# Kernel tuning notes

Hardware: AMD Instinct MI355X
Metric: run time of the kernel (lower is better)

The kernel has to match this reference:

```python
import jax, jax.numpy as jnp
import numpy as np

B, C, H, W = 4, 256, 64, 64
CH = C // 2  # inner channels of the non-local block


def _conv1x1(x, w, b):
    # 1x1 conv == channel-mixing einsum; x: [B,C,H,W], w: [O,C], b: [O]
    return jnp.einsum('oc,bchw->bohw', w, x) + b[None, :, None, None]


def setup_inputs() -> dict:
    key = jax.random.key(0)
    ks = jax.random.split(key, 9)
    s = 0.02  # small init so exp(scores) stays in fp32 range (no max-subtraction in this block)
    return {
        'x':  jax.random.normal(ks[0], (B, C, H, W), dtype=jnp.float32),
        'w1': s * jax.random.normal(ks[1], (CH, C), dtype=jnp.float32),
        'b1': jnp.zeros((CH,), jnp.float32),
        'w2': s * jax.random.normal(ks[2], (CH, C), dtype=jnp.float32),
        'b2': jnp.zeros((CH,), jnp.float32),
        'w3': s * jax.random.normal(ks[3], (CH, C), dtype=jnp.float32),
        'b3': jnp.zeros((CH,), jnp.float32),
        'w4': s * jax.random.normal(ks[4], (C, CH), dtype=jnp.float32),
        'b4': jnp.zeros((C,), jnp.float32),
    }


def reference(x, w1, b1, w2, b2, w3, b3, w4, b4):
    b, c, h, w = x.shape
    n = h * w
    theta = _conv1x1(x, w1, b1).reshape(b, -1, n)  # [B, C/2, N]
    phi   = _conv1x1(x, w2, b2).reshape(b, -1, n)  # [B, C/2, N]
    g     = _conv1x1(x, w3, b3).reshape(b, -1, n)  # [B, C/2, N]
    # full non-local affinity: [B, N, N]
    scores = jnp.einsum('bci,bcj->bij', theta, phi)
    attn = jnp.exp(scores)  # faithful: no max-subtraction in the original
    attn = attn / jnp.sum(attn, axis=1, keepdims=True)  # normalize over dim=1 as written
    y = jnp.einsum('bij,bcj->bci', attn, g)  # [B, C/2, N]
    y = y.reshape(b, -1, h, w)               # [B, C/2, H, W]
    out = _conv1x1(y, w4, b4) + x            # project back to C, residual
    return out
```

## Files before the change

kernel.cpp:

```cpp
#include <hip/hip_runtime.h>

#define DEVI __device__ __forceinline__

typedef __attribute__((ext_vector_type(8))) short bf16x8;
typedef __attribute__((ext_vector_type(4))) short bf16x4;
typedef __attribute__((ext_vector_type(4))) float f32x4;

#define MFMA16 __builtin_amdgcn_mfma_f32_16x16x32_bf16

DEVI short f2bs(float f) {
  union { float f; unsigned u; } v; v.f = f;
  unsigned r = v.u + 0x7fffu + ((v.u >> 16) & 1u);
  return (short)(r >> 16);
}
DEVI float bs2f(short s) {
  union { unsigned u; float f; } v; v.u = ((unsigned)(unsigned short)s) << 16;
  return v.f;
}

DEVI void gload_lds16(const short* g, short* lds) {
  __builtin_amdgcn_global_load_lds(
      (const __attribute__((address_space(1))) unsigned int*)g,
      (__attribute__((address_space(3))) unsigned int*)lds, 16, 0, 0);
}

DEVI void stage_chunk(short* lds, const short* g, int ldg, int tid) {
#pragma unroll
  for (int it = 0; it < 2; ++it) {
    int slot = it * 256 + tid;
    int row  = slot >> 2;
    int ko   = (slot & 3) << 3;
    gload_lds16(g + (size_t)row * ldg + ko, lds + slot * 8);
  }
}

DEVI void stage_chunk64(short* lds, const short* g, int ldg, int tid) {
  int row = tid >> 2, ko = (tid & 3) << 3;
  gload_lds16(g + (size_t)row * ldg + ko, lds + tid * 8);
}

DEVI bf16x8 lds8(const short* p) { return *(const bf16x8*)p; }

DEVI void zero_acc(f32x4 (&a)[4][4]) {
  f32x4 z = {0.f, 0.f, 0.f, 0.f};
#pragma unroll
  for (int i = 0; i < 4; ++i)
#pragma unroll
    for (int j = 0; j < 4; ++j) a[i][j] = z;
}

__global__ __launch_bounds__(256) void k_transpose_cast(const float* __restrict__ x,
                                                        short* __restrict__ xt) {
  __shared__ float t[64][65];
  int b = blockIdx.z;
  int c0 = blockIdx.y * 64;
  int p0 = blockIdx.x * 64;
  int tid = threadIdx.x;
  const float* xb = x + (size_t)b * 256 * 4096;
#pragma unroll
  for (int i = 0; i < 16; ++i) {
    int idx = i * 256 + tid;
    int c = idx >> 6, p = idx & 63;
    t[p][c] = xb[(size_t)(c0 + c) * 4096 + p0 + p];
  }
  __syncthreads();
  short* xtb = xt + ((size_t)b * 4096 + p0) * 256 + c0;
#pragma unroll
  for (int i = 0; i < 16; ++i) {
    int idx = i * 256 + tid;
    int p = idx >> 6, c = idx & 63;
    xtb[(size_t)p * 256 + c] = f2bs(t[p][c]);
  }
}

__global__ __launch_bounds__(256) void k_cast_w(const float* __restrict__ w1,
                                                const float* __restrict__ w2,
                                                const float* __restrict__ w3,
                                                short* __restrict__ w123) {
  int i = blockIdx.x * 256 + threadIdx.x;
  if (i < 384 * 256) {
    int r = i >> 8;
    const float* w = (r < 128) ? w1 : (r < 256 ? w2 : w3);
    w123[i] = f2bs(w[(size_t)(r & 127) * 256 + (i & 255)]);
  }
}

__global__ __launch_bounds__(256) void k_proj(const short* __restrict__ xt,
                                              const short* __restrict__ w123,
                                              const float* __restrict__ b1,
                                              const float* __restrict__ b2,
                                              const float* __restrict__ b3,
                                              short* __restrict__ theta,
                                              short* __restrict__ phi,
                                              short* __restrict__ gbuf) {
  __shared__ short aL[128 * 32];
  __shared__ short bL[128 * 32];
  __shared__ short oL[128 * 136];
  int tid = threadIdx.x;
  int m0 = blockIdx.x * 128;
  int nb = blockIdx.y;
  int b  = blockIdx.z;
  int lane = tid & 63, wid = tid >> 6;
  int col = lane & 15, quad = lane >> 4;
  int wm = (wid >> 1) * 64, wn = (wid & 1) * 64;
  const short* A = xt + ((size_t)b * 4096 + m0) * 256;
  const short* B = w123 + (size_t)nb * 128 * 256;
  f32x4 acc[4][4];
  zero_acc(acc);
  for (int ks = 0; ks < 8; ++ks) {
    __syncthreads();
    stage_chunk(aL, A + ks * 32, 256, tid);
    stage_chunk(bL, B + ks * 32, 256, tid);
    __syncthreads();
    bf16x8 af[4], bf_[4];
#pragma unroll
    for (int mi = 0; mi < 4; ++mi) af[mi] = lds8(&aL[(wm + mi * 16 + col) * 32 + quad * 8]);
#pragma unroll
    for (int ni = 0; ni < 4; ++ni) bf_[ni] = lds8(&bL[(wn + ni * 16 + col) * 32 + quad * 8]);
#pragma unroll
    for (int mi = 0; mi < 4; ++mi)
#pragma unroll
      for (int ni = 0; ni < 4; ++ni)
        acc[mi][ni] = MFMA16(af[mi], bf_[ni], acc[mi][ni], 0, 0, 0);
  }
  const float* bias = (nb == 0) ? b1 : (nb == 1 ? b2 : b3);
  __syncthreads();
#pragma unroll
  for (int mi = 0; mi < 4; ++mi)
#pragma unroll
    for (int ni = 0; ni < 4; ++ni) {
      float bv = bias[wn + ni * 16 + col];
#pragma unroll
      for (int r = 0; r < 4; ++r)
        oL[(wm + mi * 16 + quad * 4 + r) * 136 + wn + ni * 16 + col] = f2bs(acc[mi][ni][r] + bv);
    }
  __syncthreads();
  short* O = ((nb == 0) ? theta : (nb == 1) ? phi : gbuf) + ((size_t)b * 4096 + m0) * 128;
#pragma unroll
  for (int it = 0; it < 8; ++it) {
    int slot = it * 256 + tid;
    int r = slot >> 4, cp = (slot & 15) * 8;
    *(bf16x8*)(O + (size_t)r * 128 + cp) = lds8(&oL[r * 136 + cp]);
  }
}

__global__ __launch_bounds__(256, 2) void k_denom(const short* __restrict__ theta,
                                                  const short* __restrict__ phi,
                                                  float* __restrict__ dpart) {
  __shared__ short phB[2][16384];
  __shared__ float part[1024];
  int tid = threadIdx.x;
  int ib = blockIdx.x, jc = blockIdx.y, b = blockIdx.z;
  int lane = tid & 63, wid = tid >> 6;
  int col = lane & 15, quad = lane >> 4;
  int wm = (wid >> 1) * 64, wn = (wid & 1) * 64;
  const short* T = theta + ((size_t)b * 4096 + ib * 128) * 128;
  const short* P = phi + ((size_t)b * 4096 + (size_t)jc * 1024) * 128;
  short* Lb = &phB[0][0];
#pragma unroll
  for (int ks = 0; ks < 4; ++ks) stage_chunk(Lb + ks * 8192, T + ks * 32, 128, tid);
  __syncthreads();
  bf16x8 ath[4][4];
#pragma unroll
  for (int ks = 0; ks < 4; ++ks)
#pragma unroll
    for (int mi = 0; mi < 4; ++mi)
      ath[ks][mi] = lds8(&Lb[ks * 8192 + (wm + mi * 16 + col) * 32 + quad * 8]);
  __syncthreads();
#pragma unroll
  for (int ks = 0; ks < 4; ++ks) stage_chunk(&phB[0][0] + ks * 4096, P + ks * 32, 128, tid);
  for (int jt = 0; jt < 8; ++jt) {
    int cur = jt & 1;
    __syncthreads();
    if (jt < 7) {
      const short* Pn = P + (size_t)(jt + 1) * 128 * 128;
#pragma unroll
      for (int ks = 0; ks < 4; ++ks) stage_chunk(&phB[cur ^ 1][0] + ks * 4096, Pn + ks * 32, 128, tid);
    }
    f32x4 sacc[4][4];
    zero_acc(sacc);
#pragma unroll
    for (int ks = 0; ks < 4; ++ks) {
      bf16x8 bp[4];
#pragma unroll
      for (int ni = 0; ni < 4; ++ni) bp[ni] = lds8(&phB[cur][ks * 4096 + (wn + ni * 16 + col) * 32 + quad * 8]);
#pragma unroll
      for (int mi = 0; mi < 4; ++mi)
#pragma unroll
        for (int ni = 0; ni < 4; ++ni)
          sacc[mi][ni] = MFMA16(ath[ks][mi], bp[ni], sacc[mi][ni], 0, 0, 0);
    }
#pragma unroll
    for (int ni = 0; ni < 4; ++ni) {
      float s = 0.f;
#pragma unroll
      for (int mi = 0; mi < 4; ++mi)
#pragma unroll
        for (int r = 0; r < 4; ++r) s += __expf(sacc[mi][ni][r]);
      part[((wid >> 1) * 4 + quad) * 128 + wn + ni * 16 + col] = s;
    }
    __syncthreads();
    if (tid < 128) {
      float d = 0.f;
#pragma unroll
      for (int q = 0; q < 8; ++q) d += part[q * 128 + tid];
      dpart[((size_t)(b * 32 + ib)) * 4096 + jc * 1024 + jt * 128 + tid] = d;
    }
  }
}

__global__ __launch_bounds__(256) void k_fold(const short* __restrict__ gbuf,
                                              const float* __restrict__ dpart,
                                              short* __restrict__ gprime) {
  __shared__ float dinv[128];
  __shared__ short t[128 * 136];
  int tid = threadIdx.x;
  int jb = blockIdx.x, b = blockIdx.y;
  int j0 = jb * 128;
  if (tid < 128) {
    float d = 0.f;
    for (int ib = 0; ib < 32; ++ib) d += dpart[((size_t)(b * 32 + ib)) * 4096 + j0 + tid];
    dinv[tid] = 1.0f / d;
  }
  __syncthreads();
  const short* G = gbuf + ((size_t)b * 4096 + j0) * 128;
#pragma unroll
  for (int it = 0; it < 8; ++it) {
    int slot = it * 256 + tid;
    int j = slot >> 4, c8 = (slot & 15) * 8;
    bf16x8 gv = *(const bf16x8*)(G + (size_t)j * 128 + c8);
    float di = dinv[j];
#pragma unroll
    for (int e = 0; e < 8; ++e) t[(c8 + e) * 136 + j] = f2bs(bs2f(gv[e]) * di);
  }
  __syncthreads();
  short* GP = gprime + (size_t)b * 128 * 4096 + j0;
#pragma unroll
  for (int it = 0; it < 8; ++it) {
    int slot = it * 256 + tid;
    int c = slot >> 4, j8 = (slot & 15) * 8;
    *(bf16x8*)(GP + (size_t)c * 4096 + j8) = *(const bf16x8*)&t[c * 136 + j8];
  }
}

__global__ __launch_bounds__(256, 2) void k_attn_pv(const short* __restrict__ theta,
                                                    const short* __restrict__ phi,
                                                    const short* __restrict__ gprime,
                                                    short* __restrict__ ypart) {
  __shared__ short L[40960];
  int tid = threadIdx.x;
  int ib = blockIdx.x, jc = blockIdx.y, b = blockIdx.z;
  int lane = tid & 63, wid = tid >> 6;
  int col = lane & 15, quad = lane >> 4;
  int wm = (wid >> 1) * 64;
  int wnS = (wid & 1) * 32;
  int wnV = (wid & 1) * 64;
  const short* T = theta + ((size_t)b * 4096 + ib * 128) * 128;
  const short* PH = phi + ((size_t)b * 4096 + (size_t)jc * 1024) * 128;
  const short* GP = gprime + (size_t)b * 128 * 4096 + jc * 1024;
  short* pP = L + 32768;
#pragma unroll
  for (int ks = 0; ks < 4; ++ks) stage_chunk(L + ks * 8192, T + ks * 32, 128, tid);
  __syncthreads();
  bf16x8 ath[4][4];
#pragma unroll
  for (int ks = 0; ks < 4; ++ks)
#pragma unroll
    for (int mi = 0; mi < 4; ++mi)
      ath[ks][mi] = lds8(&L[ks * 8192 + (wm + mi * 16 + col) * 32 + quad * 8]);
  __syncthreads();
#pragma unroll
  for (int ks = 0; ks < 4; ++ks) stage_chunk64(L + ks * 2048, PH + ks * 32, 128, tid);
#pragma unroll
  for (int jh = 0; jh < 2; ++jh) stage_chunk(L + 16384 + jh * 4096, GP + jh * 32, 4096, tid);
  f32x4 accy[4][4];
  zero_acc(accy);
  for (int jt = 0; jt < 16; ++jt) {
    int cur = jt & 1;
    short* phc = L + cur * 8192;
    short* phn = L + (cur ^ 1) * 8192;
    short* gpc = L + 16384 + cur * 8192;
    short* gpn = L + 16384 + (cur ^ 1) * 8192;
    __syncthreads();
    if (jt < 15) {
      const short* PHn = PH + (size_t)(jt + 1) * 64 * 128;
#pragma unroll
      for (int ks = 0; ks < 4; ++ks) stage_chunk64(phn + ks * 2048, PHn + ks * 32, 128, tid);
    }
    f32x4 s[4][2];
#pragma unroll
    for (int mi = 0; mi < 4; ++mi)
#pragma unroll
      for (int ni = 0; ni < 2; ++ni) s[mi][ni] = (f32x4){0.f, 0.f, 0.f, 0.f};
#pragma unroll
    for (int ks = 0; ks < 4; ++ks) {
      bf16x8 bp[2];
#pragma unroll
      for (int ni = 0; ni < 2; ++ni) bp[ni] = lds8(&phc[ks * 2048 + (wnS + ni * 16 + col) * 32 + quad * 8]);
#pragma unroll
      for (int mi = 0; mi < 4; ++mi)
#pragma unroll
        for (int ni = 0; ni < 2; ++ni)
          s[mi][ni] = MFMA16(ath[ks][mi], bp[ni], s[mi][ni], 0, 0, 0);
    }
#pragma unroll
    for (int mi = 0; mi < 4; ++mi)
#pragma unroll
      for (int ni = 0; ni < 2; ++ni) {
        int jj = wnS + ni * 16 + col;
        int cj = jj >> 5, jg = (jj >> 3) & 3, jl = jj & 7;
#pragma unroll
        for (int r = 0; r < 4; ++r) {
          int i = wm + mi * 16 + quad * 4 + r;
          pP[cj * 4096 + i * 32 + (((jg ^ (i >> 2)) & 3) << 3) + jl] = f2bs(__expf(s[mi][ni][r]));
        }
      }
    __syncthreads();
    if (jt < 15) {
      const short* GPn = GP + (jt + 1) * 64;
#pragma unroll
      for (int jh = 0; jh < 2; ++jh) stage_chunk(gpn + jh * 4096, GPn + jh * 32, 4096, tid);
    }
#pragma unroll
    for (int ks = 0; ks < 2; ++ks) {
      bf16x8 ap[4], bg[4];
#pragma unroll
      for (int mi = 0; mi < 4; ++mi) {
        int i = wm + mi * 16 + col;
        ap[mi] = lds8(&pP[ks * 4096 + i * 32 + (((quad ^ (i >> 2)) & 3) << 3)]);
      }
#pragma unroll
      for (int ni = 0; ni < 4; ++ni) bg[ni] = lds8(&gpc[ks * 4096 + (wnV + ni * 16 + col) * 32 + quad * 8]);
#pragma unroll
      for (int mi = 0; mi < 4; ++mi)
#pragma unroll
        for (int ni = 0; ni < 4; ++ni)
          accy[mi][ni] = MFMA16(ap[mi], bg[ni], accy[mi][ni], 0, 0, 0);
    }
  }
  short* Yp = ypart + ((size_t)(jc * 4 + b) * 4096 + (size_t)ib * 128) * 128;
#pragma unroll
  for (int half = 0; half < 2; ++half) {
    __syncthreads();
    if ((wid >> 1) == half) {
#pragma unroll
      for (int mi = 0; mi < 4; ++mi)
#pragma unroll
        for (int ni = 0; ni < 4; ++ni)
#pragma unroll
          for (int r = 0; r < 4; ++r)
            pP[(mi * 16 + quad * 4 + r) * 128 + wnV + ni * 16 + col] = f2bs(accy[mi][ni][r]);
    }
    __syncthreads();
#pragma unroll
    for (int it = 0; it < 4; ++it) {
      int slot = it * 256 + tid;
      int r = slot >> 4, c8 = (slot & 15) * 8;
      *(bf16x8*)(Yp + (size_t)(half * 64 + r) * 128 + c8) = lds8(&pP[r * 128 + c8]);
    }
  }
}

__global__ __launch_bounds__(256) void k_out(const short* __restrict__ ypart,
                                             const float* __restrict__ w4,
                                             const float* __restrict__ b4,
                                             const float* __restrict__ x,
                                             float* __restrict__ out) {
  __shared__ short wL[4 * 4096];
  __shared__ short yL[4 * 4096];
  __shared__ float bLs[128];
  int tid = threadIdx.x;
  int ibk = blockIdx.x, ob = blockIdx.y, b = blockIdx.z;
  int o0 = ob * 128, i0 = ibk * 128;
  int lane = tid & 63, wid = tid >> 6;
  int col = lane & 15, quad = lane >> 4;
  int wm = (wid >> 1) * 64, wn = (wid & 1) * 64;
#pragma unroll
  for (int it = 0; it < 16; ++it) {
    int slot = it * 256 + tid;
    int r = slot >> 5, c4 = (slot & 31) * 4;
    int ks = c4 >> 5, cr = c4 & 31;
    f32x4 wv = *(const f32x4*)(w4 + (size_t)(o0 + r) * 128 + c4);
    bf16x4 wp;
#pragma unroll
    for (int e = 0; e < 4; ++e) wp[e] = f2bs(wv[e]);
    *(bf16x4*)&wL[ks * 4096 + r * 32 + cr] = wp;
  }
#pragma unroll
  for (int it = 0; it < 8; ++it) {
    int slot = it * 256 + tid;
    int r = slot >> 4, c8 = (slot & 15) * 8;
    int ks = c8 >> 5, cr = c8 & 31;
    float a8[8];
#pragma unroll
    for (int e = 0; e < 8; ++e) a8[e] = 0.f;
#pragma unroll
    for (int p = 0; p < 4; ++p) {
      bf16x8 v = *(const bf16x8*)(ypart + ((size_t)(p * 4 + b) * 4096 + i0 + r) * 128 + c8);
#pragma unroll
      for (int e = 0; e < 8; ++e) a8[e] += bs2f(v[e]);
    }
    bf16x8 yv;
#pragma unroll
    for (int e = 0; e < 8; ++e) yv[e] = f2bs(a8[e]);
    *(bf16x8*)&yL[ks * 4096 + r * 32 + cr] = yv;
  }
  if (tid < 128) bLs[tid] = b4[o0 + tid];
  __syncthreads();
  f32x4 acc[4][4];
  zero_acc(acc);
#pragma unroll
  for (int ks = 0; ks < 4; ++ks) {
    bf16x8 af[4], bf_[4];
#pragma unroll
    for (int mi = 0; mi < 4; ++mi) af[mi] = lds8(&wL[ks * 4096 + (wm + mi * 16 + col) * 32 + quad * 8]);
#pragma unroll
    for (int ni = 0; ni < 4; ++ni) bf_[ni] = lds8(&yL[ks * 4096 + (wn + ni * 16 + col) * 32 + quad * 8]);
#pragma unroll
    for (int mi = 0; mi < 4; ++mi)
#pragma unroll
      for (int ni = 0; ni < 4; ++ni)
        acc[mi][ni] = MFMA16(af[mi], bf_[ni], acc[mi][ni], 0, 0, 0);
  }
  const float* X = x + ((size_t)b * 256 + o0) * 4096 + i0;
  float* O = out + ((size_t)b * 256 + o0) * 4096 + i0;
#pragma unroll
  for (int mi = 0; mi < 4; ++mi)
#pragma unroll
    for (int ni = 0; ni < 4; ++ni)
#pragma unroll
      for (int r = 0; r < 4; ++r) {
        int o = wm + mi * 16 + quad * 4 + r;
        int i = wn + ni * 16 + col;
        O[(size_t)o * 4096 + i] = acc[mi][ni][r] + X[(size_t)o * 4096 + i] + bLs[o];
      }
}

extern "C" void kernel_launch(void* const* d_in, const int* in_sizes, int n_in,
                              void* d_out, int out_size, void* d_ws, size_t ws_size,
                              hipStream_t stream) {
  const float* x  = (const float*)d_in[0];
  const float* w1 = (const float*)d_in[1];
  const float* b1 = (const float*)d_in[2];
  const float* w2 = (const float*)d_in[3];
  const float* b2 = (const float*)d_in[4];
  const float* w3 = (const float*)d_in[5];
  const float* b3 = (const float*)d_in[6];
  const float* w4 = (const float*)d_in[7];
  const float* b4 = (const float*)d_in[8];
  char* ws = (char*)d_ws;
  short* xt     = (short*)(ws + 0);
  short* w123   = (short*)(ws + 8388608);
  short* theta  = (short*)(ws + 8585216);
  short* phi    = (short*)(ws + 12779520);
  short* gbuf   = (short*)(ws + 16973824);
  short* gprime = (short*)(ws + 21168128);
  float* dpart  = (float*)(ws + 25362432);
  short* ypart  = (short*)(ws + 27459584);
  float* out    = (float*)d_out;
  (void)in_sizes; (void)n_in; (void)out_size; (void)ws_size;

  k_transpose_cast<<<dim3(64, 4, 4), dim3(256), 0, stream>>>(x, xt);
  k_cast_w<<<dim3(384), dim3(256), 0, stream>>>(w1, w2, w3, w123);
  k_proj<<<dim3(32, 3, 4), dim3(256), 0, stream>>>(xt, w123, b1, b2, b3, theta, phi, gbuf);
  k_denom<<<dim3(32, 4, 4), dim3(256), 0, stream>>>(theta, phi, dpart);
  k_fold<<<dim3(32, 4), dim3(256), 0, stream>>>(gbuf, dpart, gprime);
  k_attn_pv<<<dim3(32, 4, 4), dim3(256), 0, stream>>>(theta, phi, gprime, ypart);
  k_out<<<dim3(32, 2, 4), dim3(256), 0, stream>>>(ypart, w4, b4, x, out);
}
```

Baseline: 174.9 us.

## Fuse prep kernels, drop fold pass, apply column normalization inside attention

Merges the input transpose-cast and the weight cast into one launch. The projection kernel now writes g already transposed, so the separate fold kernel goes away. The denominator kernel reduces column sums with warp shuffles and atomically accumulates into a small zeroed buffer instead of writing per-block partials. The attention kernel reads those sums and scales exp(scores) by their reciprocal before the PV matmul. The aim is fewer launches and less intermediate traffic, at the cost of atomics, a memset, and extra per-tile normalization work and barriers in the attention loop.

```diff
diff --git a/kernel.cpp b/kernel.cpp
--- a/kernel.cpp
+++ b/kernel.cpp
@@ -49,13 +49,26 @@
     for (int j = 0; j < 4; ++j) a[i][j] = z;
 }
 
-__global__ __launch_bounds__(256) void k_transpose_cast(const float* __restrict__ x,
-                                                        short* __restrict__ xt) {
+__global__ __launch_bounds__(256) void k_prep(const float* __restrict__ x,
+                                              const float* __restrict__ w1,
+                                              const float* __restrict__ w2,
+                                              const float* __restrict__ w3,
+                                              short* __restrict__ xt,
+                                              short* __restrict__ w123) {
+  int tid = threadIdx.x;
+  if (blockIdx.y == 4) {
+    int lin = blockIdx.z * 64 + blockIdx.x;
+    for (int i = lin * 256 + tid; i < 384 * 256; i += 65536) {
+      int r = i >> 8;
+      const float* w = (r < 128) ? w1 : (r < 256 ? w2 : w3);
+      w123[i] = f2bs(w[(size_t)(r & 127) * 256 + (i & 255)]);
+    }
+    return;
+  }
   __shared__ float t[64][65];
   int b = blockIdx.z;
   int c0 = blockIdx.y * 64;
   int p0 = blockIdx.x * 64;
-  int tid = threadIdx.x;
   const float* xb = x + (size_t)b * 256 * 4096;
 #pragma unroll
   for (int i = 0; i < 16; ++i) {
@@ -70,18 +83,6 @@
     int idx = i * 256 + tid;
     int p = idx >> 6, c = idx & 63;
     xtb[(size_t)p * 256 + c] = f2bs(t[p][c]);
-  }
-}
-
-__global__ __launch_bounds__(256) void k_cast_w(const float* __restrict__ w1,
-                                                const float* __restrict__ w2,
-                                                const float* __restrict__ w3,
-                                                short* __restrict__ w123) {
-  int i = blockIdx.x * 256 + threadIdx.x;
-  if (i < 384 * 256) {
-    int r = i >> 8;
-    const float* w = (r < 128) ? w1 : (r < 256 ? w2 : w3);
-    w123[i] = f2bs(w[(size_t)(r & 127) * 256 + (i & 255)]);
   }
 }
 
@@ -92,7 +93,7 @@
                                               const float* __restrict__ b3,
                                               short* __restrict__ theta,
                                               short* __restrict__ phi,
-                                              short* __restrict__ gbuf) {
+                                              short* __restrict__ gT) {
   __shared__ short aL[128 * 32];
   __shared__ short bL[128 * 32];
   __shared__ short oL[128 * 136];
@@ -125,231 +126,222 @@
   }
   const float* bias = (nb == 0) ? b1 : (nb == 1 ? b2 : b3);
   __syncthreads();
-#pragma unroll
-  for (int mi = 0; mi < 4; ++mi)
-#pragma unroll
-    for (int ni = 0; ni < 4; ++ni) {
-      float bv = bias[wn + ni * 16 + col];
-#pragma unroll
-      for (int r = 0; r < 4; ++r)
-        oL[(wm + mi * 16 + quad * 4 + r) * 136 + wn + ni * 16 + col] = f2bs(acc[mi][ni][r] + bv);
-    }
-  __syncthreads();
-  short* O = ((nb == 0) ? theta : (nb == 1) ? phi : gbuf) + ((size_t)b * 4096 + m0) * 128;
-#pragma unroll
-  for (int it = 0; it < 8; ++it) {
-    int slot = it * 256 + tid;
-    int r = slot >> 4, cp = (slot & 15) * 8;
-    *(bf16x8*)(O + (size_t)r * 128 + cp) = lds8(&oL[r * 136 + cp]);
+  if (nb < 2) {
+#pragma unroll
+    for (int mi = 0; mi < 4; ++mi)
+#pragma unroll
+      for (int ni = 0; ni < 4; ++ni) {
+        float bv = bias[wn + ni * 16 + col];
+#pragma unroll
+        for (int r = 0; r < 4; ++r)
+          oL[(wm + mi * 16 + quad * 4 + r) * 136 + wn + ni * 16 + col] = f2bs(acc[mi][ni][r] + bv);
+      }
+    __syncthreads();
+    short* O = ((nb == 0) ? theta : phi) + ((size_t)b * 4096 + m0) * 128;
+#pragma unroll
+    for (int it = 0; it < 8; ++it) {
+      int slot = it * 256 + tid;
+      int r = slot >> 4, cp = (slot & 15) * 8;
+      *(bf16x8*)(O + (size_t)r * 128 + cp) = lds8(&oL[r * 136 + cp]);
+    }
+  } else {
+#pragma unroll
+    for (int mi = 0; mi < 4; ++mi)
+#pragma unroll
+      for (int ni = 0; ni < 4; ++ni) {
+        float bv = bias[wn + ni * 16 + col];
+#pragma unroll
+        for (int r = 0; r < 4; ++r)
+          oL[(wn + ni * 16 + col) * 136 + wm + mi * 16 + quad * 4 + r] = f2bs(acc[mi][ni][r] + bv);
+      }
+    __syncthreads();
+    short* O = gT + (size_t)b * 128 * 4096 + m0;
+#pragma unroll
+    for (int it = 0; it < 8; ++it) {
+      int slot = it * 256 + tid;
+      int c = slot >> 4, p8 = (slot & 15) * 8;
+      *(bf16x8*)(O + (size_t)c * 4096 + p8) = lds8(&oL[c * 136 + p8]);
+    }
   }
 }
 
 __global__ __launch_bounds__(256, 2) void k_denom(const short* __restrict__ theta,
                                                   const short* __restrict__ phi,
-                                                  float* __restrict__ dpart) {
-  __shared__ short phB[2][16384];
-  __shared__ float part[1024];
+                                                  float* __restrict__ dsum) {
+  __shared__ short L[16384];
   int tid = threadIdx.x;
   int ib = blockIdx.x, jc = blockIdx.y, b = blockIdx.z;
   int lane = tid & 63, wid = tid >> 6;
   int col = lane & 15, quad = lane >> 4;
-  int wm = (wid >> 1) * 64, wn = (wid & 1) * 64;
-  const short* T = theta + ((size_t)b * 4096 + ib * 128) * 128;
-  const short* P = phi + ((size_t)b * 4096 + (size_t)jc * 1024) * 128;
-  short* Lb = &phB[0][0];
-#pragma unroll
-  for (int ks = 0; ks < 4; ++ks) stage_chunk(Lb + ks * 8192, T + ks * 32, 128, tid);
-  __syncthreads();
-  bf16x8 ath[4][4];
+  int wmj = (wid & 1) * 32;
+  int wni = (wid >> 1) * 64;
+  const short* TH = theta + ((size_t)b * 4096 + ib * 128) * 128;
+  const short* PH = phi + ((size_t)b * 4096 + (size_t)jc * 1024) * 128;
+  float* D = dsum + b * 4096 + jc * 1024;
+#pragma unroll
+  for (int ks = 0; ks < 4; ++ks) stage_chunk(L + ks * 4096, TH + ks * 32, 128, tid);
+  __syncthreads();
+  bf16x8 bth[4][4];
 #pragma unroll
   for (int ks = 0; ks < 4; ++ks)
 #pragma unroll
-    for (int mi = 0; mi < 4; ++mi)
-      ath[ks][mi] = lds8(&Lb[ks * 8192 + (wm + mi * 16 + col) * 32 + quad * 8]);
-  __syncthreads();
-#pragma unroll
-  for (int ks = 0; ks < 4; ++ks) stage_chunk(&phB[0][0] + ks * 4096, P + ks * 32, 128, tid);
-  for (int jt = 0; jt < 8; ++jt) {
-    int cur = jt & 1;
-    __syncthreads();
-    if (jt < 7) {
-      const short* Pn = P + (size_t)(jt + 1) * 128 * 128;
-#pragma unroll
-      for (int ks = 0; ks < 4; ++ks) stage_chunk(&phB[cur ^ 1][0] + ks * 4096, Pn + ks * 32, 128, tid);
-    }
-    f32x4 sacc[4][4];
-    zero_acc(sacc);
+    for (int ni = 0; ni < 4; ++ni)
+      bth[ks][ni] = lds8(&L[ks * 4096 + (wni + ni * 16 + col) * 32 + quad * 8]);
+  __syncthreads();
+#pragma unroll
+  for (int ks = 0; ks < 4; ++ks) stage_chunk64(L + ks * 2048, PH + ks * 32, 128, tid);
+  for (int jt = 0; jt < 16; ++jt) {
+    short* phc = L + (jt & 1) * 8192;
+    short* phn = L + ((jt & 1) ^ 1) * 8192;
+    __syncthreads();
+    if (jt < 15) {
+      const short* PHn = PH + (size_t)(jt + 1) * 64 * 128;
+#pragma unroll
+      for (int ks = 0; ks < 4; ++ks) stage_chunk64(phn + ks * 2048, PHn + ks * 32, 128, tid);
+    }
+    f32x4 s[2][4];
+#pragma unroll
+    for (int mi = 0; mi < 2; ++mi)
+#pragma unroll
+      for (int ni = 0; ni < 4; ++ni) s[mi][ni] = (f32x4){0.f, 0.f, 0.f, 0.f};
 #pragma unroll
     for (int ks = 0; ks < 4; ++ks) {
-      bf16x8 bp[4];
-#pragma unroll
-      for (int ni = 0; ni < 4; ++ni) bp[ni] = lds8(&phB[cur][ks * 4096 + (wn + ni * 16 + col) * 32 + quad * 8]);
-#pragma unroll
-      for (int mi = 0; mi < 4; ++mi)
+      bf16x8 ap[2];
+#pragma unroll
+      for (int mi = 0; mi < 2; ++mi) ap[mi] = lds8(&phc[ks * 2048 + (wmj + mi * 16 + col) * 32 + quad * 8]);
+#pragma unroll
+      for (int mi = 0; mi < 2; ++mi)
 #pragma unroll
         for (int ni = 0; ni < 4; ++ni)
-          sacc[mi][ni] = MFMA16(ath[ks][mi], bp[ni], sacc[mi][ni], 0, 0, 0);
-    }
-#pragma unroll
-    for (int ni = 0; ni < 4; ++ni) {
-      float s = 0.f;
-#pragma unroll
-      for (int mi = 0; mi < 4; ++mi)
-#pragma unroll
-        for (int r = 0; r < 4; ++r) s += __expf(sacc[mi][ni][r]);
-      part[((wid >> 1) * 4 + quad) * 128 + wn + ni * 16 + col] = s;
-    }
-    __syncthreads();
-    if (tid < 128) {
-      float d = 0.f;
-#pragma unroll
-      for (int q = 0; q < 8; ++q) d += part[q * 128 + tid];
-      dpart[((size_t)(b * 32 + ib)) * 4096 + jc * 1024 + jt * 128 + tid] = d;
-    }
-  }
-}
-
-__global__ __launch_bounds__(256) void k_fold(const short* __restrict__ gbuf,
-                                              const float* __restrict__ dpart,
-                                              short* __restrict__ gprime) {
-  __shared__ float dinv[128];
-  __shared__ short t[128 * 136];
-  int tid = threadIdx.x;
-  int jb = blockIdx.x, b = blockIdx.y;
-  int j0 = jb * 128;
-  if (tid < 128) {
-    float d = 0.f;
-    for (int ib = 0; ib < 32; ++ib) d += dpart[((size_t)(b * 32 + ib)) * 4096 + j0 + tid];
-    dinv[tid] = 1.0f / d;
-  }
-  __syncthreads();
-  const short* G = gbuf + ((size_t)b * 4096 + j0) * 128;
-#pragma unroll
-  for (int it = 0; it < 8; ++it) {
-    int slot = it * 256 + tid;
-    int j = slot >> 4, c8 = (slot & 15) * 8;
-    bf16x8 gv = *(const bf16x8*)(G + (size_t)j * 128 + c8);
-    float di = dinv[j];
-#pragma unroll
-    for (int e = 0; e < 8; ++e) t[(c8 + e) * 136 + j] = f2bs(bs2f(gv[e]) * di);
-  }
-  __syncthreads();
-  short* GP = gprime + (size_t)b * 128 * 4096 + j0;
-#pragma unroll
-  for (int it = 0; it < 8; ++it) {
-    int slot = it * 256 + tid;
-    int c = slot >> 4, j8 = (slot & 15) * 8;
-    *(bf16x8*)(GP + (size_t)c * 4096 + j8) = *(const bf16x8*)&t[c * 136 + j8];
-  }
-}
-
-__global__ __launch_bounds__(256, 2) void k_attn_pv(const short* __restrict__ theta,
-                                                    const short* __restrict__ phi,
-                                                    const short* __restrict__ gprime,
-                                                    short* __restrict__ ypart) {
-  __shared__ short L[40960];
+          s[mi][ni] = MFMA16(ap[mi], bth[ks][ni], s[mi][ni], 0, 0, 0);
+    }
+#pragma unroll
+    for (int mi = 0; mi < 2; ++mi)
+#pragma unroll
+      for (int r = 0; r < 4; ++r) {
+        float ps = __expf(s[mi][0][r]) + __expf(s[mi][1][r]) +
+                   __expf(s[mi][2][r]) + __expf(s[mi][3][r]);
+        ps += __shfl_xor(ps, 1, 16);
+        ps += __shfl_xor(ps, 2, 16);
+        ps += __shfl_xor(ps, 4, 16);
+        ps += __shfl_xor(ps, 8, 16);
+        if (col == 0) atomicAdd(D + jt * 64 + wmj + mi * 16 + quad * 4 + r, ps);
+      }
+  }
+}
+
+__global__ __launch_bounds__(256, 2) void k_attn(const short* __restrict__ theta,
+                                                 const short* __restrict__ phi,
+                                                 const short* __restrict__ gT,
+                                                 const float* __restrict__ dsum,
+                                                 short* __restrict__ ypart) {
+  __shared__ short L[33280];
   int tid = threadIdx.x;
   int ib = blockIdx.x, jc = blockIdx.y, b = blockIdx.z;
   int lane = tid & 63, wid = tid >> 6;
   int col = lane & 15, quad = lane >> 4;
-  int wm = (wid >> 1) * 64;
-  int wnS = (wid & 1) * 32;
-  int wnV = (wid & 1) * 64;
-  const short* T = theta + ((size_t)b * 4096 + ib * 128) * 128;
+  int wmj = (wid & 1) * 32;
+  int wni = (wid >> 1) * 64;
+  int wmi = (wid >> 1) * 64;
+  int wnc = (wid & 1) * 64;
+  const short* TH = theta + ((size_t)b * 4096 + ib * 128) * 128;
   const short* PH = phi + ((size_t)b * 4096 + (size_t)jc * 1024) * 128;
-  const short* GP = gprime + (size_t)b * 128 * 4096 + jc * 1024;
-  short* pP = L + 32768;
-#pragma unroll
-  for (int ks = 0; ks < 4; ++ks) stage_chunk(L + ks * 8192, T + ks * 32, 128, tid);
-  __syncthreads();
-  bf16x8 ath[4][4];
+  const short* GT = gT + (size_t)b * 128 * 4096 + jc * 1024;
+  const float* DS = dsum + b * 4096 + jc * 1024;
+  short* ph = L;
+  short* gp0 = L + 8192;
+  short* gp1 = L + 16384;
+  short* pP = L + 24576;
+#pragma unroll
+  for (int ks = 0; ks < 4; ++ks) stage_chunk(L + ks * 4096, TH + ks * 32, 128, tid);
+  __syncthreads();
+  bf16x8 bth[4][4];
 #pragma unroll
   for (int ks = 0; ks < 4; ++ks)
 #pragma unroll
-    for (int mi = 0; mi < 4; ++mi)
-      ath[ks][mi] = lds8(&L[ks * 8192 + (wm + mi * 16 + col) * 32 + quad * 8]);
-  __syncthreads();
-#pragma unroll
-  for (int ks = 0; ks < 4; ++ks) stage_chunk64(L + ks * 2048, PH + ks * 32, 128, tid);
-#pragma unroll
-  for (int jh = 0; jh < 2; ++jh) stage_chunk(L + 16384 + jh * 4096, GP + jh * 32, 4096, tid);
+    for (int ni = 0; ni < 4; ++ni)
+      bth[ks][ni] = lds8(&L[ks * 4096 + (wni + ni * 16 + col) * 32 + quad * 8]);
+  __syncthreads();
+#pragma unroll
+  for (int ks = 0; ks < 4; ++ks) stage_chunk64(ph + ks * 2048, PH + ks * 32, 128, tid);
+#pragma unroll
+  for (int s = 0; s < 2; ++s) stage_chunk(gp0 + s * 4096, GT + s * 32, 4096, tid);
   f32x4 accy[4][4];
   zero_acc(accy);
   for (int jt = 0; jt < 16; ++jt) {
-    int cur = jt & 1;
-    short* phc = L + cur * 8192;
-    short* phn = L + (cur ^ 1) * 8192;
-    short* gpc = L + 16384 + cur * 8192;
-    short* gpn = L + 16384 + (cur ^ 1) * 8192;
+    short* gpc = (jt & 1) ? gp1 : gp0;
+    short* gpn = (jt & 1) ? gp0 : gp1;
+    f32x4 dv[2];
+#pragma unroll
+    for (int mi = 0; mi < 2; ++mi)
+      dv[mi] = *(const f32x4*)(DS + jt * 64 + wmj + mi * 16 + quad * 4);
+    __syncthreads();
+    f32x4 s[2][4];
+#pragma unroll
+    for (int mi = 0; mi < 2; ++mi)
+#pragma unroll
+      for (int ni = 0; ni < 4; ++ni) s[mi][ni] = (f32x4){0.f, 0.f, 0.f, 0.f};
+#pragma unroll
+    for (int ks = 0; ks < 4; ++ks) {
+      bf16x8 ap[2];
+#pragma unroll
+      for (int mi = 0; mi < 2; ++mi) ap[mi] = lds8(&ph[ks * 2048 + (wmj + mi * 16 + col) * 32 + quad * 8]);
+#pragma unroll
+      for (int mi = 0; mi < 2; ++mi)
+#pragma unroll
+        for (int ni = 0; ni < 4; ++ni)
+          s[mi][ni] = MFMA16(ap[mi], bth[ks][ni], s[mi][ni], 0, 0, 0);
+    }
+#pragma unroll
+    for (int mi = 0; mi < 2; ++mi) {
+      int j0 = wmj + mi * 16 + quad * 4;
+      f32x4 rc;
+#pragma unroll
+      for (int r = 0; r < 4; ++r) rc[r] = __builtin_amdgcn_rcpf(dv[mi][r]);
+#pragma unroll
+      for (int ni = 0; ni < 4; ++ni) {
+        int i = wni + ni * 16 + col;
+        bf16x4 pv;
+#pragma unroll
+        for (int r = 0; r < 4; ++r) pv[r] = f2bs(__expf(s[mi][ni][r]) * rc[r]);
+        *(bf16x4*)(pP + i * 68 + j0) = pv;
+      }
+    }
     __syncthreads();
     if (jt < 15) {
       const short* PHn = PH + (size_t)(jt + 1) * 64 * 128;
 #pragma unroll
-      for (int ks = 0; ks < 4; ++ks) stage_chunk64(phn + ks * 2048, PHn + ks * 32, 128, tid);
-    }
-    f32x4 s[4][2];
-#pragma unroll
-    for (int mi = 0; mi < 4; ++mi)
-#pragma unroll
-      for (int ni = 0; ni < 2; ++ni) s[mi][ni] = (f32x4){0.f, 0.f, 0.f, 0.f};
-#pragma unroll
-    for (int ks = 0; ks < 4; ++ks) {
-      bf16x8 bp[2];
-#pragma unroll
-      for (int ni = 0; ni < 2; ++ni) bp[ni] = lds8(&phc[ks * 2048 + (wnS + ni * 16 + col) * 32 + quad * 8]);
+      for (int ks = 0; ks < 4; ++ks) stage_chunk64(ph + ks * 2048, PHn + ks * 32, 128, tid);
+      const short* GTn = GT + (jt + 1) * 64;
+#pragma unroll
+      for (int s2 = 0; s2 < 2; ++s2) stage_chunk(gpn + s2 * 4096, GTn + s2 * 32, 4096, tid);
+    }
+#pragma unroll
+    for (int ksj = 0; ksj < 2; ++ksj) {
+      bf16x8 ap2[4], bg[4];
+#pragma unroll
+      for (int mi = 0; mi < 4; ++mi) ap2[mi] = lds8(&pP[(wmi + mi * 16 + col) * 68 + ksj * 32 + quad * 8]);
+#pragma unroll
+      for (int ni = 0; ni < 4; ++ni) bg[ni] = lds8(&gpc[ksj * 4096 + (wnc + ni * 16 + col) * 32 + quad * 8]);
 #pragma unroll
       for (int mi = 0; mi < 4; ++mi)
 #pragma unroll
-        for (int ni = 0; ni < 2; ++ni)
-          s[mi][ni] = MFMA16(ath[ks][mi], bp[ni], s[mi][ni], 0, 0, 0);
-    }
-#pragma unroll
-    for (int mi = 0; mi < 4; ++mi)
-#pragma unroll
-      for (int ni = 0; ni < 2; ++ni) {
-        int jj = wnS + ni * 16 + col;
-        int cj = jj >> 5, jg = (jj >> 3) & 3, jl = jj & 7;
-#pragma unroll
-        for (int r = 0; r < 4; ++r) {
-          int i = wm + mi * 16 + quad * 4 + r;
-          pP[cj * 4096 + i * 32 + (((jg ^ (i >> 2)) & 3) << 3) + jl] = f2bs(__expf(s[mi][ni][r]));
-        }
-      }
-    __syncthreads();
-    if (jt < 15) {
-      const short* GPn = GP + (jt + 1) * 64;
-#pragma unroll
-      for (int jh = 0; jh < 2; ++jh) stage_chunk(gpn + jh * 4096, GPn + jh * 32, 4096, tid);
-    }
-#pragma unroll
-    for (int ks = 0; ks < 2; ++ks) {
-      bf16x8 ap[4], bg[4];
-#pragma unroll
-      for (int mi = 0; mi < 4; ++mi) {
-        int i = wm + mi * 16 + col;
-        ap[mi] = lds8(&pP[ks * 4096 + i * 32 + (((quad ^ (i >> 2)) & 3) << 3)]);
-      }
-#pragma unroll
-      for (int ni = 0; ni < 4; ++ni) bg[ni] = lds8(&gpc[ks * 4096 + (wnV + ni * 16 + col) * 32 + quad * 8]);
+        for (int ni = 0; ni < 4; ++ni)
+          accy[mi][ni] = MFMA16(ap2[mi], bg[ni], accy[mi][ni], 0, 0, 0);
+    }
+  }
+  short* Yp = ypart + ((size_t)(jc * 4 + b) * 4096 + (size_t)ib * 128) * 128;
+#pragma unroll
+  for (int half = 0; half < 2; ++half) {
+    __syncthreads();
+    if ((wid >> 1) == half) {
 #pragma unroll
       for (int mi = 0; mi < 4; ++mi)
 #pragma unroll
         for (int ni = 0; ni < 4; ++ni)
-          accy[mi][ni] = MFMA16(ap[mi], bg[ni], accy[mi][ni], 0, 0, 0);
-    }
-  }
-  short* Yp = ypart + ((size_t)(jc * 4 + b) * 4096 + (size_t)ib * 128) * 128;
-#pragma unroll
-  for (int half = 0; half < 2; ++half) {
-    __syncthreads();
-    if ((wid >> 1) == half) {
-#pragma unroll
-      for (int mi = 0; mi < 4; ++mi)
-#pragma unroll
-        for (int ni = 0; ni < 4; ++ni)
 #pragma unroll
           for (int r = 0; r < 4; ++r)
-            pP[(mi * 16 + quad * 4 + r) * 128 + wnV + ni * 16 + col] = f2bs(accy[mi][ni][r]);
+            pP[(mi * 16 + quad * 4 + r) * 128 + wnc + ni * 16 + col] = f2bs(accy[mi][ni][r]);
     }
     __syncthreads();
 #pragma unroll
@@ -449,22 +441,20 @@
   const float* w4 = (const float*)d_in[7];
   const float* b4 = (const float*)d_in[8];
   char* ws = (char*)d_ws;
-  short* xt     = (short*)(ws + 0);
-  short* w123   = (short*)(ws + 8388608);
-  short* theta  = (short*)(ws + 8585216);
-  short* phi    = (short*)(ws + 12779520);
-  short* gbuf   = (short*)(ws + 16973824);
-  short* gprime = (short*)(ws + 21168128);
-  float* dpart  = (float*)(ws + 25362432);
-  short* ypart  = (short*)(ws + 27459584);
-  float* out    = (float*)d_out;
+  short* xt    = (short*)(ws + 0);
+  short* w123  = (short*)(ws + 8388608);
+  short* theta = (short*)(ws + 8585216);
+  short* phi   = (short*)(ws + 12779520);
+  short* gT    = (short*)(ws + 16973824);
+  float* dsum  = (float*)(ws + 21168128);
+  short* ypart = (short*)(ws + 21233664);
+  float* out   = (float*)d_out;
   (void)in_sizes; (void)n_in; (void)out_size; (void)ws_size;
 
-  k_transpose_cast<<<dim3(64, 4, 4), dim3(256), 0, stream>>>(x, xt);
-  k_cast_w<<<dim3(384), dim3(256), 0, stream>>>(w1, w2, w3, w123);
-  k_proj<<<dim3(32, 3, 4), dim3(256), 0, stream>>>(xt, w123, b1, b2, b3, theta, phi, gbuf);
-  k_denom<<<dim3(32, 4, 4), dim3(256), 0, stream>>>(theta, phi, dpart);
-  k_fold<<<dim3(32, 4), dim3(256), 0, stream>>>(gbuf, dpart, gprime);
-  k_attn_pv<<<dim3(32, 4, 4), dim3(256), 0, stream>>>(theta, phi, gprime, ypart);
+  hipMemsetAsync(dsum, 0, 4 * 4096 * sizeof(float), stream);
+  k_prep<<<dim3(64, 5, 4), dim3(256), 0, stream>>>(x, w1, w2, w3, xt, w123);
+  k_proj<<<dim3(32, 3, 4), dim3(256), 0, stream>>>(xt, w123, b1, b2, b3, theta, phi, gT);
+  k_denom<<<dim3(32, 4, 4), dim3(256), 0, stream>>>(theta, phi, dsum);
+  k_attn<<<dim3(32, 4, 4), dim3(256), 0, stream>>>(theta, phi, gT, dsum, ypart);
   k_out<<<dim3(32, 2, 4), dim3(256), 0, stream>>>(ypart, w4, b4, x, out);
 }
```

Result: slower. 247.0 us (+41.2%).
